# Performance work log

Hardware: AMD Instinct MI355X
Metric: run time of the kernel (lower is better)

## Reference

```python
import jax, jax.numpy as jnp
import numpy as np

IN_BIT = 8      # in_bit_width
W_BIT = 2       # weight_bit_width (also output act quantizer bit width)
BN_EPS = 1e-4


def _ste(x, q):
    # straight-through estimator: forward = q, backward = identity w.r.t. x
    return x + jax.lax.stop_gradient(q - x)


def act_quant(x, bit):
    # CommonActQuant: signed int quant, narrow_range=False, power-of-two scale
    # range [-1, 1 - 2^{-(bit-1)}] -> scale = 2^{-(bit-1)}
    s = 2.0 ** (1 - bit)
    n_min = -(2.0 ** (bit - 1))
    n_max = 2.0 ** (bit - 1) - 1.0
    q = jnp.clip(jnp.round(x / s), n_min, n_max) * s
    return _ste(x, q)


def weight_quant(w, bit):
    # CommonWeightQuant: narrow-range signed int quant, unit scaling const
    # scale = 1 / (2^{bit-1} - 1); for bit=2 levels are {-1, 0, 1}
    n = 2.0 ** (bit - 1) - 1.0
    s = 1.0 / n
    q = jnp.clip(jnp.round(w / s), -n, n) * s
    return _ste(w, q)


def setup_inputs() -> dict:
    key = jax.random.key(0)
    k1, k2, k3, k4 = jax.random.split(key, 4)
    B, C, H, W = 32, 256, 32, 32
    x = jax.random.normal(k1, (B, C, H, W), dtype=jnp.float32) * 0.5
    weight = jax.random.normal(k2, (C, C, 3, 3), dtype=jnp.float32) * 0.5
    gamma = jnp.ones((C,), dtype=jnp.float32)
    beta = jnp.zeros((C,), dtype=jnp.float32)
    running_mean = jax.random.normal(k3, (C,), dtype=jnp.float32) * 0.1
    running_var = jax.random.uniform(k4, (C,), dtype=jnp.float32, minval=0.5, maxval=1.5)
    return {"x": x, "weight": weight, "gamma": gamma, "beta": beta,
            "running_mean": running_mean, "running_var": running_var}


def reference(x, weight, gamma, beta, running_mean, running_var):
    # 1) input QuantIdentity (8-bit, [-1, 1-2^-7], power-of-two scale 2^-7)
    xq = act_quant(x, IN_BIT)
    # 2) QuantConv2d 3x3 stride 1 pad 1, no bias, 2-bit weights
    wq = weight_quant(weight, W_BIT)
    y = jax.lax.conv_general_dilated(
        xq, wq, window_strides=(1, 1), padding=((1, 1), (1, 1)),
        dimension_numbers=("NCHW", "OIHW", "NCHW"))
    # 3) BatchNorm2d (inference, eps=1e-4)
    inv = gamma / jnp.sqrt(running_var + BN_EPS)
    y = y * inv[None, :, None, None] + (beta - running_mean * inv)[None, :, None, None]
    # 4) output QuantIdentity at weight_bit_width bits
    return act_quant(y, W_BIT)
```

## Files before the change

kernel.cpp:

```cpp
#include <hip/hip_runtime.h>
#include <hip/hip_bf16.h>
#include <stdint.h>


typedef int i32x4 __attribute__((ext_vector_type(4)));
typedef float f32x4 __attribute__((ext_vector_type(4)));

__global__ __launch_bounds__(256) void wquant_kernel(
    const float* __restrict__ w, signed char* __restrict__ wq)
{
    __shared__ signed char wt[9 * 256];
    const int t = threadIdx.x;
    const int co = blockIdx.x;
#pragma unroll
    for (int p = 0; p < 9; ++p) {
        const int idx = p * 256 + t;
        const float v = w[co * 2304 + idx];
        const int ci = idx / 9;
        const int khkw = idx - 9 * ci;
        const float q = fminf(fmaxf(rintf(v), -1.f), 1.f);
        wt[khkw * 256 + ci] = (signed char)(int)q;
    }
    __syncthreads();
    if (t < 144) {
        const int kt = t >> 2, kq = t & 3;
        const uint4 v = *(const uint4*)(wt + t * 16);
        *(uint4*)(wq + ((size_t)((co >> 4) * 36 + kt) << 10) + kq * 256 + (co & 15) * 16) = v;
    }
}

__global__ __launch_bounds__(512, 4) void conv_gemm_kernel(
    const float* __restrict__ x, const signed char* __restrict__ wqm,
    const float* __restrict__ gamma, const float* __restrict__ beta,
    const float* __restrict__ mean, const float* __restrict__ var,
    float* __restrict__ out)
{
    __shared__ signed char As[6 * 34 * 256];

    const int tid = threadIdx.x;
    const int wv = tid >> 6;
    const int lane = tid & 63;
    const int l16 = lane & 15;
    const int l4 = lane >> 4;

    const int bid = (int)blockIdx.x;
    const int swz = (bid & 7) * 64 + (bid >> 3);

    const int mt = swz >> 1;
    const int n0 = (swz & 1) * 128;
    const int b = mt >> 3;
    const int h0 = (mt & 7) * 4;
    const int wave_m = wv & 1;
    const int wave_n = wv >> 1;

    const signed char* bp0 = wqm + (((size_t)((n0 >> 4) + wave_n * 2 + 0) * 36) << 10) + lane * 16;
    const signed char* bp1 = wqm + (((size_t)((n0 >> 4) + wave_n * 2 + 1) * 36) << 10) + lane * 16;

    i32x4 aP[2][4], bP[3][2];

#define LOAD_B(kt, dst) { dst[0] = *(const i32x4*)(bp0 + (kt) * 1024); \
                          dst[1] = *(const i32x4*)(bp1 + (kt) * 1024); }
#define LOAD_A(kt, dst) { const int khkw = (kt) >> 2; \
                          const int kh = khkw / 3; \
                          const int kw = khkw - 3 * kh; \
                          const int roff = kh * 34 + kw; \
                          const int cb = ((kt) & 3) * 4 + l4; \
                          _Pragma("unroll") \
                          for (int i = 0; i < 4; ++i) { \
                              const int r = r0[i] + roff; \
                              dst[i] = *(const i32x4*)(As + r * 256 + ((cb ^ (r & 15)) << 4)); \
                          } }
#define MFMA(af, bf) { _Pragma("unroll") \
                       for (int i = 0; i < 4; ++i) \
                           _Pragma("unroll") \
                           for (int j = 0; j < 2; ++j) \
                               acc[i][j] = __builtin_amdgcn_mfma_i32_16x16x64_i8(af[i], bf[j], acc[i][j], 0, 0, 0); }

    LOAD_B(0, bP[0])
    LOAD_B(1, bP[1])

    const uint4 z = {0u, 0u, 0u, 0u};
    if (tid < 192) {
        const int pair = tid >> 4;
        const int hh = pair >> 1;
        const int wp = (pair & 1) * 33;
        const bool covered = (h0 == 0 && hh == 0) || (h0 == 28 && hh == 5);
        if (!covered) {
            const int r = hh * 34 + wp;
            const int ch = tid & 15;
            *(uint4*)(As + r * 256 + ((ch ^ (r & 15)) << 4)) = z;
        }
    }
    if (h0 == 0) {
        for (int i = tid; i < 544; i += 512) {
            const int r = i >> 4;
            const int ch = i & 15;
            *(uint4*)(As + r * 256 + ((ch ^ (r & 15)) << 4)) = z;
        }
    }
    if (h0 == 28) {
        for (int i = tid; i < 544; i += 512) {
            const int r = 5 * 34 + (i >> 4);
            const int ch = i & 15;
            *(uint4*)(As + r * 256 + ((ch ^ (r & 15)) << 4)) = z;
        }
    }

    const int cib = tid >> 3;
    const int w4 = tid & 7;
#pragma unroll
    for (int hh = 0; hh < 6; ++hh) {
        const int h = h0 + hh - 1;
        if (h < 0 || h > 31) continue;
        const float* xb = x + ((size_t)(b * 256) * 32 + h) * 32;
        unsigned row[4];
#pragma unroll
        for (int j = 0; j < 4; ++j) {
            const f32x4 v = *(const f32x4*)(xb + (size_t)(cib * 4 + j) * 1024 + w4 * 4);
            unsigned p = 0;
#pragma unroll
            for (int k = 0; k < 4; ++k) {
                const float q = fminf(fmaxf(rintf(__fmul_rn(v[k], 128.f)), -128.f), 127.f);
                p |= ((unsigned)(unsigned char)(signed char)(int)q) << (8 * k);
            }
            row[j] = p;
        }
        const unsigned ab_lo = __builtin_amdgcn_perm(row[1], row[0], 0x05010400u);
        const unsigned ab_hi = __builtin_amdgcn_perm(row[1], row[0], 0x07030602u);
        const unsigned cd_lo = __builtin_amdgcn_perm(row[3], row[2], 0x05010400u);
        const unsigned cd_hi = __builtin_amdgcn_perm(row[3], row[2], 0x07030602u);
        unsigned col[4];
        col[0] = __builtin_amdgcn_perm(cd_lo, ab_lo, 0x05040100u);
        col[1] = __builtin_amdgcn_perm(cd_lo, ab_lo, 0x07060302u);
        col[2] = __builtin_amdgcn_perm(cd_hi, ab_hi, 0x05040100u);
        col[3] = __builtin_amdgcn_perm(cd_hi, ab_hi, 0x07060302u);
#pragma unroll
        for (int r = 0; r < 4; ++r) {
            const int rr = hh * 34 + w4 * 4 + r + 1;
            *(unsigned*)(As + rr * 256 + (((cib >> 2) ^ (rr & 15)) << 4) + (cib & 3) * 4) = col[r];
        }
    }
    __syncthreads();

    int r0[4];
#pragma unroll
    for (int i = 0; i < 4; ++i)
        r0[i] = (wave_m * 2 + (i >> 1)) * 34 + (i & 1) * 16 + l16;

    i32x4 acc[4][2];
#pragma unroll
    for (int i = 0; i < 4; i++)
#pragma unroll
        for (int j = 0; j < 2; j++) acc[i][j] = (i32x4){0, 0, 0, 0};

    LOAD_A(0, aP[0])
#pragma unroll
    for (int kt = 0; kt < 36; ++kt) {
        if (kt + 2 < 36) { LOAD_B(kt + 2, bP[(kt + 2) % 3]) }
        if (kt + 1 < 36) { LOAD_A(kt + 1, aP[(kt + 1) & 1]) }
        MFMA(aP[kt & 1], bP[kt % 3])
    }

#pragma unroll
    for (int j = 0; j < 2; ++j) {
        const int co = n0 + wave_n * 32 + j * 16 + l16;
        const float iv = __fdiv_rn(gamma[co], __fsqrt_rn(__fadd_rn(var[co], 1e-4f)));
        const float bias = __fsub_rn(beta[co], __fmul_rn(mean[co], iv));
#pragma unroll
        for (int i = 0; i < 4; ++i) {
            const int h = h0 + wave_m * 2 + (i >> 1);
            const int w = (i & 1) * 16 + l4 * 4;
            f32x4 v;
#pragma unroll
            for (int r = 0; r < 4; r++) {
                const float y = __fmul_rn((float)acc[i][j][r], 0.0078125f);
                const float t = __fadd_rn(__fmul_rn(y, iv), bias);
                float z2 = rintf(__fmul_rn(t, 2.f));
                z2 = fminf(fmaxf(z2, -2.f), 1.f);
                v[r] = __fmul_rn(z2, 0.5f);
            }
            *(f32x4*)(&out[(((size_t)(b * 256 + co)) * 32 + h) * 32 + w]) = v;
        }
    }
#undef LOAD_B
#undef LOAD_A
#undef MFMA
}

extern "C" void kernel_launch(void* const* d_in, const int* in_sizes, int n_in,
                              void* d_out, int out_size, void* d_ws, size_t ws_size,
                              hipStream_t stream) {
    const float* x      = (const float*)d_in[0];
    const float* weight = (const float*)d_in[1];
    const float* gamma  = (const float*)d_in[2];
    const float* beta   = (const float*)d_in[3];
    const float* rmean  = (const float*)d_in[4];
    const float* rvar   = (const float*)d_in[5];
    float* out = (float*)d_out;

    signed char* wq = (signed char*)d_ws;

    wquant_kernel<<<256, 256, 0, stream>>>(weight, wq);
    conv_gemm_kernel<<<512, 512, 0, stream>>>(x, wq, gamma, beta, rmean, rvar, out);
}
```

Before: 113.6 us.

## Switch int8 conv GEMM from 16x16x64 to 32x32x32 MFMA tiles

Replaces the 4x2 grid of 16x16x64 int8 MFMAs per wave with 2 accumulators of 32x32x32 MFMAs. The weight pre-layout, A-fragment LDS loads and epilogue indexing are reworked to match the new operand and accumulator layouts. Larger MFMA tiles cut LDS fragment traffic per MAC and may give better matrix-core throughput. The cost is a new accumulator-to-output mapping, different LDS access patterns and possible bank conflicts.

```diff
diff --git a/kernel.cpp b/kernel.cpp
--- a/kernel.cpp
+++ b/kernel.cpp
@@ -4,6 +4,7 @@
 
 
 typedef int i32x4 __attribute__((ext_vector_type(4)));
+typedef int i32x16 __attribute__((ext_vector_type(16)));
 typedef float f32x4 __attribute__((ext_vector_type(4)));
 
 __global__ __launch_bounds__(256) void wquant_kernel(
@@ -25,7 +26,8 @@
     if (t < 144) {
         const int kt = t >> 2, kq = t & 3;
         const uint4 v = *(const uint4*)(wt + t * 16);
-        *(uint4*)(wq + ((size_t)((co >> 4) * 36 + kt) << 10) + kq * 256 + (co & 15) * 16) = v;
+        *(uint4*)(wq + (((size_t)(co >> 5) * 72 + kt * 2 + (kq >> 1)) << 10)
+                     + (((kq & 1) << 5) + (co & 31)) * 16) = v;
     }
 }
 
@@ -40,8 +42,8 @@
     const int tid = threadIdx.x;
     const int wv = tid >> 6;
     const int lane = tid & 63;
-    const int l16 = lane & 15;
-    const int l4 = lane >> 4;
+    const int l32 = lane & 31;
+    const int lhi = lane >> 5;
 
     const int bid = (int)blockIdx.x;
     const int swz = (bid & 7) * 64 + (bid >> 3);
@@ -53,28 +55,30 @@
     const int wave_m = wv & 1;
     const int wave_n = wv >> 1;
 
-    const signed char* bp0 = wqm + (((size_t)((n0 >> 4) + wave_n * 2 + 0) * 36) << 10) + lane * 16;
-    const signed char* bp1 = wqm + (((size_t)((n0 >> 4) + wave_n * 2 + 1) * 36) << 10) + lane * 16;
-
-    i32x4 aP[2][4], bP[3][2];
-
-#define LOAD_B(kt, dst) { dst[0] = *(const i32x4*)(bp0 + (kt) * 1024); \
-                          dst[1] = *(const i32x4*)(bp1 + (kt) * 1024); }
+    const signed char* bp = wqm
+        + (((size_t)((n0 >> 5) + wave_n) * 72) << 10) + lane * 16;
+
+    i32x4 aP[2][2][2], bP[3][2];
+
+#define LOAD_B(kt, dst) { dst[0] = *(const i32x4*)(bp + ((kt) * 2 + 0) * 1024); \
+                          dst[1] = *(const i32x4*)(bp + ((kt) * 2 + 1) * 1024); }
 #define LOAD_A(kt, dst) { const int khkw = (kt) >> 2; \
                           const int kh = khkw / 3; \
                           const int kw = khkw - 3 * kh; \
                           const int roff = kh * 34 + kw; \
-                          const int cb = ((kt) & 3) * 4 + l4; \
                           _Pragma("unroll") \
-                          for (int i = 0; i < 4; ++i) { \
+                          for (int i = 0; i < 2; ++i) { \
                               const int r = r0[i] + roff; \
-                              dst[i] = *(const i32x4*)(As + r * 256 + ((cb ^ (r & 15)) << 4)); \
-                          } }
+                              _Pragma("unroll") \
+                              for (int s = 0; s < 2; ++s) { \
+                                  const int cb = ((kt) & 3) * 4 + s * 2 + lhi; \
+                                  dst[i][s] = *(const i32x4*)(As + r * 256 + ((cb ^ (r & 15)) << 4)); \
+                              } } }
 #define MFMA(af, bf) { _Pragma("unroll") \
-                       for (int i = 0; i < 4; ++i) \
+                       for (int s = 0; s < 2; ++s) \
                            _Pragma("unroll") \
-                           for (int j = 0; j < 2; ++j) \
-                               acc[i][j] = __builtin_amdgcn_mfma_i32_16x16x64_i8(af[i], bf[j], acc[i][j], 0, 0, 0); }
+                           for (int i = 0; i < 2; ++i) \
+                               acc[i] = __builtin_amdgcn_mfma_i32_32x32x32_i8(af[i][s], bf[s], acc[i], 0, 0, 0); }
 
     LOAD_B(0, bP[0])
     LOAD_B(1, bP[1])
@@ -142,16 +146,16 @@
     }
     __syncthreads();
 
-    int r0[4];
-#pragma unroll
-    for (int i = 0; i < 4; ++i)
-        r0[i] = (wave_m * 2 + (i >> 1)) * 34 + (i & 1) * 16 + l16;
-
-    i32x4 acc[4][2];
-#pragma unroll
-    for (int i = 0; i < 4; i++)
-#pragma unroll
-        for (int j = 0; j < 2; j++) acc[i][j] = (i32x4){0, 0, 0, 0};
+    int r0[2];
+#pragma unroll
+    for (int i = 0; i < 2; ++i)
+        r0[i] = (wave_m * 2 + i) * 34 + l32;
+
+    i32x16 acc[2];
+#pragma unroll
+    for (int i = 0; i < 2; i++)
+#pragma unroll
+        for (int r = 0; r < 16; r++) acc[i][r] = 0;
 
     LOAD_A(0, aP[0])
 #pragma unroll
@@ -161,19 +165,19 @@
         MFMA(aP[kt & 1], bP[kt % 3])
     }
 
-#pragma unroll
-    for (int j = 0; j < 2; ++j) {
-        const int co = n0 + wave_n * 32 + j * 16 + l16;
-        const float iv = __fdiv_rn(gamma[co], __fsqrt_rn(__fadd_rn(var[co], 1e-4f)));
-        const float bias = __fsub_rn(beta[co], __fmul_rn(mean[co], iv));
-#pragma unroll
-        for (int i = 0; i < 4; ++i) {
-            const int h = h0 + wave_m * 2 + (i >> 1);
-            const int w = (i & 1) * 16 + l4 * 4;
+    const int co = n0 + wave_n * 32 + l32;
+    const float iv = __fdiv_rn(gamma[co], __fsqrt_rn(__fadd_rn(var[co], 1e-4f)));
+    const float bias = __fsub_rn(beta[co], __fmul_rn(mean[co], iv));
+#pragma unroll
+    for (int i = 0; i < 2; ++i) {
+        const int h = h0 + wave_m * 2 + i;
+#pragma unroll
+        for (int q = 0; q < 4; ++q) {
+            const int w = q * 8 + lhi * 4;
             f32x4 v;
 #pragma unroll
             for (int r = 0; r < 4; r++) {
-                const float y = __fmul_rn((float)acc[i][j][r], 0.0078125f);
+                const float y = __fmul_rn((float)acc[i][q * 4 + r], 0.0078125f);
                 const float t = __fadd_rn(__fmul_rn(y, iv), bias);
                 float z2 = rintf(__fmul_rn(t, 2.f));
                 z2 = fminf(fmaxf(z2, -2.f), 1.f);
```

New measurement: 128.3 us. +13.0%, slower.

## Overlap staging of last two input rows with first kernel-row MFMAs

Applied to the files above, without the earlier changes.

The input halo tile is now staged in two phases. Rows 0-3 are quantized into shared memory before the first barrier. The global loads for rows 4-5 are issued early into registers, and those rows are quantized and written only after the first barrier, while the kh=0 MFMAs run. A second barrier before kt=12 makes the later rows visible. This aims to hide global-load and quantization latency behind tensor work, at the cost of 32 extra VGPRs under a tight 512x4 launch bound.

```diff
diff --git a/kernel.cpp b/kernel.cpp
--- a/kernel.cpp
+++ b/kernel.cpp
@@ -75,9 +75,43 @@
                            _Pragma("unroll") \
                            for (int j = 0; j < 2; ++j) \
                                acc[i][j] = __builtin_amdgcn_mfma_i32_16x16x64_i8(af[i], bf[j], acc[i][j], 0, 0, 0); }
+#define QUANT_TR(vsrc, col) { unsigned row[4]; \
+        _Pragma("unroll") \
+        for (int j = 0; j < 4; ++j) { \
+            unsigned p = 0; \
+            _Pragma("unroll") \
+            for (int k = 0; k < 4; ++k) { \
+                const float q = fminf(fmaxf(rintf(__fmul_rn(vsrc[j][k], 128.f)), -128.f), 127.f); \
+                p |= ((unsigned)(unsigned char)(signed char)(int)q) << (8 * k); \
+            } \
+            row[j] = p; \
+        } \
+        const unsigned ab_lo = __builtin_amdgcn_perm(row[1], row[0], 0x05010400u); \
+        const unsigned ab_hi = __builtin_amdgcn_perm(row[1], row[0], 0x07030602u); \
+        const unsigned cd_lo = __builtin_amdgcn_perm(row[3], row[2], 0x05010400u); \
+        const unsigned cd_hi = __builtin_amdgcn_perm(row[3], row[2], 0x07030602u); \
+        col[0] = __builtin_amdgcn_perm(cd_lo, ab_lo, 0x05040100u); \
+        col[1] = __builtin_amdgcn_perm(cd_lo, ab_lo, 0x07060302u); \
+        col[2] = __builtin_amdgcn_perm(cd_hi, ab_hi, 0x05040100u); \
+        col[3] = __builtin_amdgcn_perm(cd_hi, ab_hi, 0x07060302u); }
 
     LOAD_B(0, bP[0])
     LOAD_B(1, bP[1])
+
+    const int cib = tid >> 3;
+    const int w4 = tid & 7;
+
+    f32x4 ph2[2][4];
+    const bool p2v1 = (h0 + 4 <= 31);
+#pragma unroll
+    for (int u = 0; u < 2; ++u) {
+        const int h = h0 + 3 + u;
+        if (u == 1 && !p2v1) continue;
+        const float* xb = x + ((size_t)(b * 256) * 32 + h) * 32;
+#pragma unroll
+        for (int j = 0; j < 4; ++j)
+            ph2[u][j] = *(const f32x4*)(xb + (size_t)(cib * 4 + j) * 1024 + w4 * 4);
+    }
 
     const uint4 z = {0u, 0u, 0u, 0u};
     if (tid < 192) {
@@ -106,34 +140,17 @@
         }
     }
 
-    const int cib = tid >> 3;
-    const int w4 = tid & 7;
-#pragma unroll
-    for (int hh = 0; hh < 6; ++hh) {
+#pragma unroll
+    for (int hh = 0; hh < 4; ++hh) {
         const int h = h0 + hh - 1;
-        if (h < 0 || h > 31) continue;
+        if (h < 0) continue;
         const float* xb = x + ((size_t)(b * 256) * 32 + h) * 32;
-        unsigned row[4];
-#pragma unroll
-        for (int j = 0; j < 4; ++j) {
-            const f32x4 v = *(const f32x4*)(xb + (size_t)(cib * 4 + j) * 1024 + w4 * 4);
-            unsigned p = 0;
-#pragma unroll
-            for (int k = 0; k < 4; ++k) {
-                const float q = fminf(fmaxf(rintf(__fmul_rn(v[k], 128.f)), -128.f), 127.f);
-                p |= ((unsigned)(unsigned char)(signed char)(int)q) << (8 * k);
-            }
-            row[j] = p;
-        }
-        const unsigned ab_lo = __builtin_amdgcn_perm(row[1], row[0], 0x05010400u);
-        const unsigned ab_hi = __builtin_amdgcn_perm(row[1], row[0], 0x07030602u);
-        const unsigned cd_lo = __builtin_amdgcn_perm(row[3], row[2], 0x05010400u);
-        const unsigned cd_hi = __builtin_amdgcn_perm(row[3], row[2], 0x07030602u);
+        f32x4 vsrc[4];
+#pragma unroll
+        for (int j = 0; j < 4; ++j)
+            vsrc[j] = *(const f32x4*)(xb + (size_t)(cib * 4 + j) * 1024 + w4 * 4);
         unsigned col[4];
-        col[0] = __builtin_amdgcn_perm(cd_lo, ab_lo, 0x05040100u);
-        col[1] = __builtin_amdgcn_perm(cd_lo, ab_lo, 0x07060302u);
-        col[2] = __builtin_amdgcn_perm(cd_hi, ab_hi, 0x05040100u);
-        col[3] = __builtin_amdgcn_perm(cd_hi, ab_hi, 0x07060302u);
+        QUANT_TR(vsrc, col)
 #pragma unroll
         for (int r = 0; r < 4; ++r) {
             const int rr = hh * 34 + w4 * 4 + r + 1;
@@ -154,8 +171,33 @@
         for (int j = 0; j < 2; j++) acc[i][j] = (i32x4){0, 0, 0, 0};
 
     LOAD_A(0, aP[0])
-#pragma unroll
-    for (int kt = 0; kt < 36; ++kt) {
+
+#pragma unroll
+    for (int u = 0; u < 2; ++u) {
+        if (u == 1 && !p2v1) continue;
+        const int hh = 4 + u;
+        unsigned col[4];
+        QUANT_TR(ph2[u], col)
+#pragma unroll
+        for (int r = 0; r < 4; ++r) {
+            const int rr = hh * 34 + w4 * 4 + r + 1;
+            *(unsigned*)(As + rr * 256 + (((cib >> 2) ^ (rr & 15)) << 4) + (cib & 3) * 4) = col[r];
+        }
+    }
+
+#pragma unroll
+    for (int kt = 0; kt < 11; ++kt) {
+        LOAD_B(kt + 2, bP[(kt + 2) % 3])
+        LOAD_A(kt + 1, aP[(kt + 1) & 1])
+        MFMA(aP[kt & 1], bP[kt % 3])
+    }
+    LOAD_B(13, bP[1])
+    MFMA(aP[1], bP[2])
+    __syncthreads();
+
+    LOAD_A(12, aP[0])
+#pragma unroll
+    for (int kt = 12; kt < 36; ++kt) {
         if (kt + 2 < 36) { LOAD_B(kt + 2, bP[(kt + 2) % 3]) }
         if (kt + 1 < 36) { LOAD_A(kt + 1, aP[(kt + 1) & 1]) }
         MFMA(aP[kt & 1], bP[kt % 3])
@@ -185,6 +227,7 @@
 #undef LOAD_B
 #undef LOAD_A
 #undef MFMA
+#undef QUANT_TR
 }
 
 extern "C" void kernel_launch(void* const* d_in, const int* in_sizes, int n_in,
```

Result: slower. 120.6 us (+6.2%).
